# Kernel optimization log

Measured on AMD Instinct MI355X. Metric: run time of the kernel, lower is better.

## Reference

```python
import jax, jax.numpy as jnp
import numpy as np

P = 30000    # pathway graph nodes
E = 480000   # edges
G = 20000    # genes
MP = 32      # max pathways per gene (padded)
R = 28       # pathway root count
B = 4096     # batch of gene pairs
IN, H, OUT = 394, 256, 64
GD = 128     # params.gene_dim


def setup_inputs() -> dict:
    key = jax.random.key(0)
    ks = iter(jax.random.split(key, 48))
    nx = lambda shape, s=1.0: jax.random.normal(next(ks), shape, dtype=jnp.float32) * s
    inp = {}
    inp["x1"] = nx((P, IN))
    inp["x2"] = nx((P, IN))
    inp["edge_src"] = jax.random.randint(next(ks), (E,), 0, P)
    inp["edge_dst"] = jax.random.randint(next(ks), (E,), 0, P)
    inp["edge_weight"] = jax.random.uniform(next(ks), (E,), dtype=jnp.float32)
    for g in ("g1", "g2"):
        inp[g + "_w1"] = nx((IN, H), 0.05); inp[g + "_b1"] = jnp.zeros((H,), jnp.float32)
        inp[g + "_w2"] = nx((H, OUT), 0.05); inp[g + "_b2"] = jnp.zeros((OUT,), jnp.float32)
    inp["pl1_w"] = nx((OUT * R, 256), 0.02); inp["pl1_b"] = jnp.zeros((256,), jnp.float32)
    inp["bn1_g"] = jnp.ones((256,), jnp.float32); inp["bn1_b"] = jnp.zeros((256,), jnp.float32)
    inp["pl2_w"] = nx((256, GD), 0.05); inp["pl2_b"] = jnp.zeros((GD,), jnp.float32)
    inp["bn2_g"] = jnp.ones((GD,), jnp.float32); inp["bn2_b"] = jnp.zeros((GD,), jnp.float32)
    inp["fc_w"] = nx((2 * GD, 256), 0.05); inp["fc_b"] = jnp.zeros((256,), jnp.float32)
    inp["fc1_w"] = nx((256, 128), 0.05); inp["fc1_b"] = jnp.zeros((128,), jnp.float32)
    inp["fc2_w"] = nx((128, 1), 0.05); inp["fc2_b"] = jnp.zeros((1,), jnp.float32)
    inp["pathway_root"] = jax.random.randint(next(ks), (P,), 0, R)
    inp["gene_paths"] = jax.random.randint(next(ks), (G, MP), 0, P)
    inp["gene_paths_mask"] = jax.random.uniform(next(ks), (G, MP)) < 0.7
    inp["head_ids"] = jax.random.randint(next(ks), (B,), 0, G)
    inp["tail_ids"] = jax.random.randint(next(ks), (B,), 0, G)
    return inp


def gcn_conv(x, w, b, src, dst, ew):
    # PyG GCNConv with edge weights + self loops (fill_value=1), symmetric norm.
    h = x @ w
    deg = jnp.zeros((x.shape[0],), x.dtype).at[dst].add(ew) + 1.0
    norm = jax.lax.rsqrt(deg)
    msg = h[src] * (ew * norm[src] * norm[dst])[:, None]
    agg = jnp.zeros_like(h).at[dst].add(msg) + h * (norm * norm)[:, None]
    return agg + b


def pathway_gcn(x, w1, b1, w2, b2, src, dst, ew):
    h = jax.nn.relu(gcn_conv(x, w1, b1, src, dst, ew))  # F.dropout in eval = identity
    return gcn_conv(h, w2, b2, src, dst, ew)


def gene_pathway_feat(s, gene_ids, gene_paths, gene_paths_mask, pathway_root):
    # Vectorized form of the per-gene python-loop gather + per-root sum.
    paths = gene_paths[gene_ids]                      # [B, MP]
    m = gene_paths_mask[gene_ids].astype(s.dtype)     # [B, MP]
    gathered = s[paths]                               # [B, MP, 64]
    oh = jax.nn.one_hot(pathway_root[paths], R, dtype=s.dtype) * m[..., None]
    feat = jnp.einsum('bpr,bpd->brd', oh, gathered)   # segment-sum into roots
    return feat.reshape(paths.shape[0], R * s.shape[1])


def batchnorm(x, g, b, eps=1e-5):
    mu = x.mean(0)
    var = x.var(0)  # biased, as torch BN training
    return g * (x - mu) * jax.lax.rsqrt(var + eps) + b


def reference(x1, x2, edge_src, edge_dst, edge_weight,
              g1_w1, g1_b1, g1_w2, g1_b2, g2_w1, g2_b1, g2_w2, g2_b2,
              pl1_w, pl1_b, bn1_g, bn1_b, pl2_w, pl2_b, bn2_g, bn2_b,
              fc_w, fc_b, fc1_w, fc1_b, fc2_w, fc2_b,
              pathway_root, gene_paths, gene_paths_mask, head_ids, tail_ids):
    out1 = pathway_gcn(x1, g1_w1, g1_b1, g1_w2, g1_b2, edge_src, edge_dst, edge_weight)
    out2 = pathway_gcn(x2, g2_w1, g2_b1, g2_w2, g2_b2, edge_src, edge_dst, edge_weight)
    s = out1 + out2  # original stacks feats from both graphs per pathway, then sums

    def fuse(ids):
        f = gene_pathway_feat(s, ids, gene_paths, gene_paths_mask, pathway_root)
        h = jax.nn.relu(batchnorm(f @ pl1_w + pl1_b, bn1_g, bn1_b))
        return batchnorm(h @ pl2_w + pl2_b, bn2_g, bn2_b)

    fuse_feat = jnp.concatenate([fuse(head_ids), fuse(tail_ids)], axis=1)  # [B, 2*GD]
    final = jax.nn.relu(fuse_feat @ fc_w + fc_b) @ fc1_w + fc1_b
    return jax.nn.relu(final) @ fc2_w + fc2_b  # [B, 1]
```

## Files before the change

kernel.cpp:

```cpp
#include <hip/hip_runtime.h>
#include <cstdint>

typedef __attribute__((ext_vector_type(4))) float f32x4;
typedef __attribute__((ext_vector_type(8))) short s16x8;

__device__ inline unsigned short f2bf(float f) {
    unsigned u = __float_as_uint(f);
    unsigned r = (u + 0x7FFFu + ((u >> 16) & 1u)) >> 16;
    return (unsigned short)r;
}
__device__ inline float b2f(unsigned short h) {
    return __uint_as_float(((unsigned)h) << 16);
}

__device__ inline void gload16(const unsigned short* g, unsigned short* l) {
    __builtin_amdgcn_global_load_lds(
        (const __attribute__((address_space(1))) unsigned int*)g,
        (__attribute__((address_space(3))) unsigned int*)l, 16, 0, 0);
}

struct TD { const float* in; unsigned short* out; int K, N, Kp, ldo; };

__global__ void prep_kernel(const unsigned char* __restrict__ mask, int maskBytes,
                            int* __restrict__ flag, float* __restrict__ zspan, long long zwords,
                            TD d0, TD d1, TD d2, TD d3, TD d4, TD d5, TD d6, TD d7) {
    int y = blockIdx.y;
    if (y == 0) {
        if (blockIdx.x != 0) return;
        __shared__ int isByte, isFloat;
        if (threadIdx.x == 0) { isByte = 0; isFloat = 0; }
        __syncthreads();
        const unsigned* w = (const unsigned*)mask;
        for (int i = threadIdx.x; i < maskBytes / 4; i += blockDim.x) {
            unsigned v = w[i];
            if (v == 0u || v == 1u) continue;
            if (v == 0x3f800000u) isFloat = 1; else isByte = 1;
        }
        __syncthreads();
        if (threadIdx.x == 0) *flag = isFloat ? 2 : (isByte ? 1 : 0);
        return;
    }
    if (y == 1) {
        long long i = (long long)blockIdx.x * 256 + threadIdx.x;
        if (i < zwords) zspan[i] = 0.f;
        return;
    }
    TD d = d0;
    if (y == 3) d = d1; else if (y == 4) d = d2; else if (y == 5) d = d3;
    else if (y == 6) d = d4; else if (y == 7) d = d5; else if (y == 8) d = d6; else if (y == 9) d = d7;
    int idx = blockIdx.x * 256 + threadIdx.x;
    if (idx >= d.N * d.Kp) return;
    int n = idx / d.Kp, k = idx - n * d.Kp;
    d.out[(size_t)n * d.ldo + k] = (k < d.K) ? f2bf(d.in[(size_t)k * d.N + n]) : (unsigned short)0;
}

__global__ void deg_cnt_kernel(const int* __restrict__ dst, const float* __restrict__ ew,
                               float* __restrict__ degw, int* __restrict__ cnt, int E) {
    int e = blockIdx.x * 256 + threadIdx.x;
    if (e >= E) return;
    int d = dst[e];
    unsafeAtomicAdd(&degw[d], ew[e]);
    atomicAdd(&cnt[d], 1);
}

__global__ __launch_bounds__(1024) void norm_scan_kernel(const int* __restrict__ cnt,
                                                         int* __restrict__ rowstart,
                                                         float* __restrict__ degw, int P) {
    int t = threadIdx.x;
    if (blockIdx.x > 0) {
        int i = (blockIdx.x - 1) * 1024 + t;
        if (i < P) degw[i] = rsqrtf(degw[i] + 1.0f);
        return;
    }
    __shared__ int wsum[16];
    __shared__ int carry;
    int lane = t & 63, w = t >> 6;
    if (t == 0) { carry = 0; rowstart[0] = 0; }
    __syncthreads();
    for (int base = 0; base < P; base += 1024) {
        int v = (base + t < P) ? cnt[base + t] : 0;
        int x = v;
#pragma unroll
        for (int off = 1; off < 64; off <<= 1) {
            int y = __shfl_up(x, off);
            if (lane >= off) x += y;
        }
        if (lane == 63) wsum[w] = x;
        __syncthreads();
        if (w == 0) {
            int xs = (lane < 16) ? wsum[lane] : 0;
#pragma unroll
            for (int off = 1; off < 16; off <<= 1) {
                int y = __shfl_up(xs, off);
                if (lane >= off) xs += y;
            }
            if (lane < 16) wsum[lane] = xs;
        }
        __syncthreads();
        int wbase = (w == 0) ? 0 : wsum[w - 1];
        int inc = carry + wbase + x;
        if (base + t < P) rowstart[base + t + 1] = inc;
        __syncthreads();
        if (t == 1023) carry = inc;
        __syncthreads();
    }
}

__global__ void fill_kernel(const int* __restrict__ src, const int* __restrict__ dst,
                            const float* __restrict__ ew, const float* __restrict__ norm,
                            const int* __restrict__ rowstart, int* __restrict__ fill,
                            int* __restrict__ csrc, float* __restrict__ coef, int E) {
    int e = blockIdx.x * 256 + threadIdx.x;
    if (e >= E) return;
    int d = dst[e], sI = src[e];
    int pos = rowstart[d] + atomicAdd(&fill[d], 1);
    csrc[pos] = sI;
    coef[pos] = ew[e] * norm[sI] * norm[d];
}

__global__ __launch_bounds__(256) void conv1_agg_kernel(
    const unsigned short* __restrict__ Hb, const float* __restrict__ norm,
    const int* __restrict__ rowstart, const int* __restrict__ csrc, const float* __restrict__ coef,
    const float* __restrict__ b0, const float* __restrict__ b1,
    unsigned short* __restrict__ out, int P) {
    int node = blockIdx.x * 4 + (threadIdx.x >> 6);
    if (node >= P) return;
    int z = blockIdx.y;
    const unsigned short* H = Hb + (size_t)z * P * 256;
    const float* bias = z ? b1 : b0;
    int lane = threadIdx.x & 63;
    int f4 = lane * 4;
    float nn = norm[node];
    ushort4 hv = *(const ushort4*)(H + (size_t)node * 256 + f4);
    float a0 = b2f(hv.x) * nn * nn, a1 = b2f(hv.y) * nn * nn;
    float a2 = b2f(hv.z) * nn * nn, a3 = b2f(hv.w) * nn * nn;
    int s0 = rowstart[node], s1 = rowstart[node + 1];
    int p = s0;
    for (; p + 4 <= s1; p += 4) {
        int i0 = csrc[p], i1 = csrc[p + 1], i2 = csrc[p + 2], i3 = csrc[p + 3];
        float c0 = coef[p], c1 = coef[p + 1], c2 = coef[p + 2], c3 = coef[p + 3];
        ushort4 v0 = *(const ushort4*)(H + (size_t)i0 * 256 + f4);
        ushort4 v1 = *(const ushort4*)(H + (size_t)i1 * 256 + f4);
        ushort4 v2 = *(const ushort4*)(H + (size_t)i2 * 256 + f4);
        ushort4 v3 = *(const ushort4*)(H + (size_t)i3 * 256 + f4);
        a0 += b2f(v0.x) * c0 + b2f(v1.x) * c1 + b2f(v2.x) * c2 + b2f(v3.x) * c3;
        a1 += b2f(v0.y) * c0 + b2f(v1.y) * c1 + b2f(v2.y) * c2 + b2f(v3.y) * c3;
        a2 += b2f(v0.z) * c0 + b2f(v1.z) * c1 + b2f(v2.z) * c2 + b2f(v3.z) * c3;
        a3 += b2f(v0.w) * c0 + b2f(v1.w) * c1 + b2f(v2.w) * c2 + b2f(v3.w) * c3;
    }
    for (; p < s1; ++p) {
        int i0 = csrc[p];
        float c0 = coef[p];
        ushort4 v0 = *(const ushort4*)(H + (size_t)i0 * 256 + f4);
        a0 += b2f(v0.x) * c0; a1 += b2f(v0.y) * c0; a2 += b2f(v0.z) * c0; a3 += b2f(v0.w) * c0;
    }
    float4 bv = *(const float4*)(bias + f4);
    ushort4 o;
    o.x = f2bf(fmaxf(a0 + bv.x, 0.f));
    o.y = f2bf(fmaxf(a1 + bv.y, 0.f));
    o.z = f2bf(fmaxf(a2 + bv.z, 0.f));
    o.w = f2bf(fmaxf(a3 + bv.w, 0.f));
    *(ushort4*)(out + (size_t)node * 512 + z * 256 + f4) = o;
}

__global__ __launch_bounds__(256) void conv2_agg_kernel(
    const unsigned short* __restrict__ T, const float* __restrict__ norm,
    const int* __restrict__ rowstart, const int* __restrict__ csrc, const float* __restrict__ coef,
    const float* __restrict__ b0, const float* __restrict__ b1,
    float* __restrict__ s, int P) {
    int node = blockIdx.x * 4 + (threadIdx.x >> 6);
    if (node >= P) return;
    int lane = threadIdx.x & 63;
    float nn = norm[node];
    float acc = b2f(T[(size_t)node * 64 + lane]) * nn * nn;
    int s0 = rowstart[node], s1 = rowstart[node + 1];
    int p = s0;
    for (; p + 4 <= s1; p += 4) {
        int i0 = csrc[p], i1 = csrc[p + 1], i2 = csrc[p + 2], i3 = csrc[p + 3];
        float c0 = coef[p], c1 = coef[p + 1], c2 = coef[p + 2], c3 = coef[p + 3];
        acc += b2f(T[(size_t)i0 * 64 + lane]) * c0 + b2f(T[(size_t)i1 * 64 + lane]) * c1 +
               b2f(T[(size_t)i2 * 64 + lane]) * c2 + b2f(T[(size_t)i3 * 64 + lane]) * c3;
    }
    for (; p < s1; ++p) acc += b2f(T[(size_t)csrc[p] * 64 + lane]) * coef[p];
    s[(size_t)node * 64 + lane] = acc + b0[lane] + b1[lane];
}

struct G2 {
    const void* A[2]; const unsigned short* Bt[2]; const float* bias[2];
    float* Cf[2]; unsigned short* Cb[2];
};

template<int BM, int BN, int WM, int WN>
__global__ __launch_bounds__(256) void gemm1_hybrid_kernel(
    const float* __restrict__ x0, const float* __restrict__ x1,
    const unsigned short* __restrict__ Bt0, const unsigned short* __restrict__ Bt1,
    unsigned short* __restrict__ C0, unsigned short* __restrict__ C1,
    int M, int IN, int Kp, int ldc) {
    const int z = blockIdx.z;
    const float* A = z ? x1 : x0;
    const unsigned short* Bt = z ? Bt1 : Bt0;
    unsigned short* Cb = z ? C1 : C0;

    constexpr int LDK = 40;
    __shared__ __align__(16) unsigned short As[BM * LDK];
    __shared__ __align__(16) unsigned short Bs[BN * 32];
    const int t = threadIdx.x, lane = t & 63, wid = t >> 6;
    constexpr int NWC = BN / WN;
    const int wr = wid / NWC, wc = wid % NWC;
    constexpr int MR = WM / 16, NR = WN / 16;
    static_assert((BM / WM) * (BN / WN) == 4, "4 waves");
    constexpr int BI = BN / 64;
    const int row0 = blockIdx.y * BM, col0 = blockIdx.x * BN;
    const int sr = lane >> 2;
    const int sc = ((lane & 3) ^ ((lane >> 3) & 3)) * 8;
    int brow[BI];
#pragma unroll
    for (int i = 0; i < BI; ++i) brow[i] = col0 + (wid * BI + i) * 16 + sr;
    const int ar = t >> 2, akc = (t & 3) * 8;
    int arowg = row0 + ar; if (arowg >= M) arowg = M - 1;
    const float* aptr = A + (size_t)arowg * IN;

    f32x4 acc[MR][NR] = {};
    const int r16 = lane & 15, q = lane >> 4;
    const int kbA = q * 8;
    const int kbB = ((q ^ ((r16 >> 1) & 3)) * 8);

    for (int kt = 0; kt < Kp; kt += 32) {
#pragma unroll
        for (int i = 0; i < BI; ++i)
            gload16(Bt + (size_t)brow[i] * Kp + kt + sc, &Bs[(wid * BI + i) * 512]);
        {
            int kg = kt + akc;
            float v[8];
            if (kg + 8 <= IN) {
                float2 a = *(const float2*)(aptr + kg);
                float2 b = *(const float2*)(aptr + kg + 2);
                float2 c = *(const float2*)(aptr + kg + 4);
                float2 d = *(const float2*)(aptr + kg + 6);
                v[0]=a.x; v[1]=a.y; v[2]=b.x; v[3]=b.y; v[4]=c.x; v[5]=c.y; v[6]=d.x; v[7]=d.y;
            } else {
#pragma unroll
                for (int j = 0; j < 8; ++j) v[j] = (kg + j < IN) ? aptr[kg + j] : 0.f;
            }
            s16x8 w;
#pragma unroll
            for (int j = 0; j < 8; ++j) w[j] = (short)f2bf(v[j]);
            *(s16x8*)&As[ar * LDK + akc] = w;
        }
        __syncthreads();
        s16x8 af[MR], bfr[NR];
#pragma unroll
        for (int m = 0; m < MR; ++m)
            af[m] = *(const s16x8*)&As[(wr * WM + m * 16 + r16) * LDK + kbA];
#pragma unroll
        for (int n = 0; n < NR; ++n)
            bfr[n] = *(const s16x8*)&Bs[(wc * WN + n * 16 + r16) * 32 + kbB];
#pragma unroll
        for (int m = 0; m < MR; ++m)
#pragma unroll
            for (int n = 0; n < NR; ++n)
                acc[m][n] = __builtin_amdgcn_mfma_f32_16x16x32_bf16(af[m], bfr[n], acc[m][n], 0, 0, 0);
        __syncthreads();
    }
#pragma unroll
    for (int m = 0; m < MR; ++m)
#pragma unroll
        for (int n = 0; n < NR; ++n) {
            int col = col0 + wc * WN + n * 16 + r16;
#pragma unroll
            for (int r = 0; r < 4; ++r) {
                int row = row0 + wr * WM + m * 16 + q * 4 + r;
                if (row < M) Cb[(size_t)row * ldc + col] = f2bf(acc[m][n][r]);
            }
        }
}

template<int BM, int BN, int WM, int WN>
__global__ __launch_bounds__(256) void m97s_gemm_kernel(
    G2 g, int M, int Kp, int lda, int ldc, int relu) {
    const int z = blockIdx.z;
    const unsigned short* A = (const unsigned short*)(z ? g.A[1] : g.A[0]);
    const unsigned short* Bt = z ? g.Bt[1] : g.Bt[0];
    const float* bias = z ? g.bias[1] : g.bias[0];
    float* Cf = z ? g.Cf[1] : g.Cf[0];
    unsigned short* Cb = z ? g.Cb[1] : g.Cb[0];

    __shared__ __align__(16) unsigned short As[BM * 32];
    __shared__ __align__(16) unsigned short Bs[BN * 32];
    const int t = threadIdx.x, lane = t & 63, wid = t >> 6;
    constexpr int NWC = BN / WN;
    const int wr = wid / NWC, wc = wid % NWC;
    constexpr int MR = WM / 16, NR = WN / 16;
    static_assert((BM / WM) * (BN / WN) == 4, "4 waves");
    constexpr int AI = BM / 64, BI = BN / 64;
    const int row0 = blockIdx.y * BM, col0 = blockIdx.x * BN;
    const int sr = lane >> 2;
    const int sc = ((lane & 3) ^ ((lane >> 3) & 3)) * 8;
    int arow[AI];
#pragma unroll
    for (int i = 0; i < AI; ++i) {
        int r = row0 + (wid * AI + i) * 16 + sr;
        arow[i] = r < M ? r : M - 1;
    }
    int brow[BI];
#pragma unroll
    for (int i = 0; i < BI; ++i) brow[i] = col0 + (wid * BI + i) * 16 + sr;

    f32x4 acc[MR][NR] = {};
    const int r16 = lane & 15;
    const int kb = (((lane >> 4) ^ ((r16 >> 1) & 3)) * 8);

    for (int kt = 0; kt < Kp; kt += 32) {
#pragma unroll
        for (int i = 0; i < AI; ++i)
            gload16(A + (size_t)arow[i] * lda + kt + sc, &As[(wid * AI + i) * 512]);
#pragma unroll
        for (int i = 0; i < BI; ++i)
            gload16(Bt + (size_t)brow[i] * Kp + kt + sc, &Bs[(wid * BI + i) * 512]);
        __syncthreads();
        s16x8 af[MR], bfr[NR];
#pragma unroll
        for (int m = 0; m < MR; ++m)
            af[m] = *(const s16x8*)&As[(wr * WM + m * 16 + r16) * 32 + kb];
#pragma unroll
        for (int n = 0; n < NR; ++n)
            bfr[n] = *(const s16x8*)&Bs[(wc * WN + n * 16 + r16) * 32 + kb];
#pragma unroll
        for (int m = 0; m < MR; ++m)
#pragma unroll
            for (int n = 0; n < NR; ++n)
                acc[m][n] = __builtin_amdgcn_mfma_f32_16x16x32_bf16(af[m], bfr[n], acc[m][n], 0, 0, 0);
        __syncthreads();
    }
#pragma unroll
    for (int m = 0; m < MR; ++m)
#pragma unroll
        for (int n = 0; n < NR; ++n) {
            int col = col0 + wc * WN + n * 16 + r16;
#pragma unroll
            for (int r = 0; r < 4; ++r) {
                int row = row0 + wr * WM + m * 16 + (lane >> 4) * 4 + r;
                if (row < M) {
                    float v = acc[m][n][r] + (bias ? bias[col] : 0.f);
                    if (relu) v = fmaxf(v, 0.f);
                    if (Cf) Cf[(size_t)row * ldc + col] = v;
                    if (Cb) Cb[(size_t)row * ldc + col] = f2bf(v);
                }
            }
        }
}

template<int BM, int BN, int WM, int WN>
__global__ __launch_bounds__(256) void pl1_stats_kernel(
    G2 g, int M, int Kp, int lda, int ldc, float* __restrict__ statsPart, int C) {
    const int z = blockIdx.z;
    const unsigned short* A = (const unsigned short*)(z ? g.A[1] : g.A[0]);
    const unsigned short* Bt = z ? g.Bt[1] : g.Bt[0];
    const float* bias = z ? g.bias[1] : g.bias[0];
    float* Cf = z ? g.Cf[1] : g.Cf[0];

    __shared__ __align__(16) unsigned short As[BM * 32];
    __shared__ __align__(16) unsigned short Bs[BN * 32];
    const int t = threadIdx.x, lane = t & 63, wid = t >> 6;
    constexpr int NWC = BN / WN;
    const int wr = wid / NWC, wc = wid % NWC;
    constexpr int MR = WM / 16, NR = WN / 16;
    constexpr int AI = BM / 64, BI = BN / 64;
    const int row0 = blockIdx.y * BM, col0 = blockIdx.x * BN;
    const int sr = lane >> 2;
    const int sc = ((lane & 3) ^ ((lane >> 3) & 3)) * 8;
    int arow[AI];
#pragma unroll
    for (int i = 0; i < AI; ++i) {
        int r = row0 + (wid * AI + i) * 16 + sr;
        arow[i] = r < M ? r : M - 1;
    }
    int brow[BI];
#pragma unroll
    for (int i = 0; i < BI; ++i) brow[i] = col0 + (wid * BI + i) * 16 + sr;

    f32x4 acc[MR][NR] = {};
    const int r16 = lane & 15, q = lane >> 4;
    const int kb = ((q ^ ((r16 >> 1) & 3)) * 8);

    for (int kt = 0; kt < Kp; kt += 32) {
#pragma unroll
        for (int i = 0; i < AI; ++i)
            gload16(A + (size_t)arow[i] * lda + kt + sc, &As[(wid * AI + i) * 512]);
#pragma unroll
        for (int i = 0; i < BI; ++i)
            gload16(Bt + (size_t)brow[i] * Kp + kt + sc, &Bs[(wid * BI + i) * 512]);
        __syncthreads();
        s16x8 af[MR], bfr[NR];
#pragma unroll
        for (int m = 0; m < MR; ++m)
            af[m] = *(const s16x8*)&As[(wr * WM + m * 16 + r16) * 32 + kb];
#pragma unroll
        for (int n = 0; n < NR; ++n)
            bfr[n] = *(const s16x8*)&Bs[(wc * WN + n * 16 + r16) * 32 + kb];
#pragma unroll
        for (int m = 0; m < MR; ++m)
#pragma unroll
            for (int n = 0; n < NR; ++n)
                acc[m][n] = __builtin_amdgcn_mfma_f32_16x16x32_bf16(af[m], bfr[n], acc[m][n], 0, 0, 0);
        __syncthreads();
    }
    float* sp = statsPart + (size_t)z * 2 * C;
#pragma unroll
    for (int n = 0; n < NR; ++n) {
        int col = col0 + wc * WN + n * 16 + r16;
        float sm = 0.f, sq = 0.f;
#pragma unroll
        for (int m = 0; m < MR; ++m)
#pragma unroll
            for (int r = 0; r < 4; ++r) {
                int row = row0 + wr * WM + m * 16 + q * 4 + r;
                float v = acc[m][n][r] + bias[col];
                Cf[(size_t)row * ldc + col] = v;
                sm += v; sq += v * v;
            }
        sm += __shfl_xor(sm, 16); sq += __shfl_xor(sq, 16);
        sm += __shfl_xor(sm, 32); sq += __shfl_xor(sq, 32);
        if (lane < 16) {
            unsafeAtomicAdd(&sp[col], sm);
            unsafeAtomicAdd(&sp[C + col], sq);
        }
    }
}

template<int BM, int BN, int WM, int WN>
__global__ __launch_bounds__(256) void pl2_bn_stats_kernel(
    const float* __restrict__ z1, const unsigned short* __restrict__ Bt,
    const float* __restrict__ bias, float* __restrict__ z2,
    const float* __restrict__ bn1part, const float* __restrict__ bn1g, const float* __restrict__ bn1b,
    float* __restrict__ bn2part, int Mrows, int Kp, int ldc) {
    const int z = blockIdx.z;
    const float* A = z1 + (size_t)z * Mrows * Kp;
    float* Cf = z2 + (size_t)z * Mrows * ldc;

    constexpr int LDK = 40;
    __shared__ __align__(16) unsigned short As[BM * LDK];
    __shared__ __align__(16) unsigned short Bs[BN * 32];
    __shared__ float sc1[256], sh1[256];
    const int t = threadIdx.x, lane = t & 63, wid = t >> 6;
    {
        const float* bp = bn1part + (size_t)z * 2 * 256;
        float mu = bp[t] / Mrows;
        float var = bp[256 + t] / Mrows - mu * mu;
        float rstd = rsqrtf(var + 1e-5f);
        float s = rstd * bn1g[t];
        sc1[t] = s; sh1[t] = bn1b[t] - mu * s;
    }
    constexpr int NWC = BN / WN;
    const int wr = wid / NWC, wc = wid % NWC;
    constexpr int MR = WM / 16, NR = WN / 16;
    constexpr int BI = BN / 64;
    const int row0 = blockIdx.y * BM, col0 = blockIdx.x * BN;
    const int sr = lane >> 2;
    const int sc = ((lane & 3) ^ ((lane >> 3) & 3)) * 8;
    int brow[BI];
#pragma unroll
    for (int i = 0; i < BI; ++i) brow[i] = col0 + (wid * BI + i) * 16 + sr;
    const int ar = t >> 2, akc = (t & 3) * 8;
    const float* aptr = A + (size_t)(row0 + ar) * Kp;
    f32x4 acc[MR][NR] = {};
    const int r16 = lane & 15, q = lane >> 4;
    const int kbA = q * 8;
    const int kbB = ((q ^ ((r16 >> 1) & 3)) * 8);
    __syncthreads();

    for (int kt = 0; kt < Kp; kt += 32) {
#pragma unroll
        for (int i = 0; i < BI; ++i)
            gload16(Bt + (size_t)brow[i] * Kp + kt + sc, &Bs[(wid * BI + i) * 512]);
        {
            int kg = kt + akc;
            float4 a = *(const float4*)(aptr + kg);
            float4 b = *(const float4*)(aptr + kg + 4);
            float v[8] = {a.x, a.y, a.z, a.w, b.x, b.y, b.z, b.w};
            s16x8 w;
#pragma unroll
            for (int j = 0; j < 8; ++j)
                w[j] = (short)f2bf(fmaxf(v[j] * sc1[kg + j] + sh1[kg + j], 0.f));
            *(s16x8*)&As[ar * LDK + akc] = w;
        }
        __syncthreads();
        s16x8 af[MR], bfr[NR];
#pragma unroll
        for (int m = 0; m < MR; ++m)
            af[m] = *(const s16x8*)&As[(wr * WM + m * 16 + r16) * LDK + kbA];
#pragma unroll
        for (int n = 0; n < NR; ++n)
            bfr[n] = *(const s16x8*)&Bs[(wc * WN + n * 16 + r16) * 32 + kbB];
#pragma unroll
        for (int m = 0; m < MR; ++m)
#pragma unroll
            for (int n = 0; n < NR; ++n)
                acc[m][n] = __builtin_amdgcn_mfma_f32_16x16x32_bf16(af[m], bfr[n], acc[m][n], 0, 0, 0);
        __syncthreads();
    }
    float* sp = bn2part + (size_t)z * 2 * ldc;
#pragma unroll
    for (int n = 0; n < NR; ++n) {
        int col = col0 + wc * WN + n * 16 + r16;
        float sm = 0.f, sq = 0.f;
#pragma unroll
        for (int m = 0; m < MR; ++m)
#pragma unroll
            for (int r = 0; r < 4; ++r) {
                int row = row0 + wr * WM + m * 16 + q * 4 + r;
                float v = acc[m][n][r] + bias[col];
                Cf[(size_t)row * ldc + col] = v;
                sm += v; sq += v * v;
            }
        sm += __shfl_xor(sm, 16); sq += __shfl_xor(sq, 16);
        sm += __shfl_xor(sm, 32); sq += __shfl_xor(sq, 32);
        if (lane < 16) {
            unsafeAtomicAdd(&sp[col], sm);
            unsafeAtomicAdd(&sp[ldc + col], sq);
        }
    }
}

__global__ __launch_bounds__(64) void gene_feat_kernel(
    const float* __restrict__ S, const int* __restrict__ head, const int* __restrict__ tail,
    const int* __restrict__ gene_paths, const void* __restrict__ mask,
    const int* __restrict__ root, unsigned short* __restrict__ feat, const int* __restrict__ flag,
    int B) {
    __shared__ float lds[28 * 64];
    int lane = threadIdx.x;
#pragma unroll
    for (int i = 0; i < 28; ++i) lds[i * 64 + lane] = 0.f;
    int side = blockIdx.y;
    const int* ids = side ? tail : head;
    int gene = ids[blockIdx.x];
    int fl = *flag;
    const unsigned char* mb = (const unsigned char*)mask;
    const int* mi = (const int*)mask;
    const float* mf = (const float*)mask;
    for (int p = 0; p < 32; ++p) {
        int idx = gene * 32 + p;
        int m = (fl == 0) ? mi[idx] : (fl == 1) ? (int)mb[idx] : (mf[idx] != 0.f);
        if (!m) continue;
        int path = gene_paths[idx];
        int r = root[path];
        lds[r * 64 + lane] += S[(size_t)path * 64 + lane];
    }
    unsigned short* frow = feat + ((size_t)side * B + blockIdx.x) * 1792;
#pragma unroll
    for (int i = 0; i < 28; ++i) frow[i * 64 + lane] = f2bf(lds[i * 64 + lane]);
}

__global__ __launch_bounds__(256) void mlp_tail_kernel(
    const float* __restrict__ z2, const float* __restrict__ bn2part,
    const float* __restrict__ bn2g, const float* __restrict__ bn2b,
    const unsigned short* __restrict__ fct, const float* __restrict__ fc_b,
    const unsigned short* __restrict__ fc1t, const float* __restrict__ fc1_b,
    const float* __restrict__ fc2_w, const float* __restrict__ fc2_b,
    float* __restrict__ out, int B) {
    constexpr int LDK = 40;
    __shared__ __align__(16) unsigned short As[64 * LDK];
    __shared__ __align__(16) unsigned short Bs[256 * 32];
    __shared__ __align__(16) unsigned short T1[64 * 264];
    __shared__ float part[64];
    __shared__ float sc2[256], sh2[256];
    const int t = threadIdx.x, lane = t & 63, wid = t >> 6;
    const int row0 = blockIdx.x * 64;
    const int sr = lane >> 2, sc = ((lane & 3) ^ ((lane >> 3) & 3)) * 8;
    const int r16 = lane & 15, q = lane >> 4;
    const int kbA = q * 8;
    const int kbB = ((q ^ ((r16 >> 1) & 3)) * 8);
    const int ar = t >> 2, akc = (t & 3) * 8;

    {
        int side = t >> 7, cc = t & 127;
        const float* bp = bn2part + (size_t)side * 256;
        float mu = bp[cc] / B;
        float var = bp[128 + cc] / B - mu * mu;
        float rstd = rsqrtf(var + 1e-5f);
        float s = rstd * bn2g[cc];
        sc2[t] = s; sh2[t] = bn2b[cc] - mu * s;
    }
    __syncthreads();

    {
        f32x4 acc[4][4] = {};
        int brow[4];
#pragma unroll
        for (int i = 0; i < 4; ++i) brow[i] = (wid * 4 + i) * 16 + sr;
        for (int kt = 0; kt < 256; kt += 32) {
#pragma unroll
            for (int i = 0; i < 4; ++i)
                gload16(fct + (size_t)brow[i] * 256 + kt + sc, &Bs[(wid * 4 + i) * 512]);
            {
                int c0 = kt + akc;
                int side = c0 >> 7, cc = c0 & 127;
                const float* zr = z2 + ((size_t)side * B + row0 + ar) * 128 + cc;
                float4 a = *(const float4*)zr;
                float4 b = *(const float4*)(zr + 4);
                float v[8] = {a.x, a.y, a.z, a.w, b.x, b.y, b.z, b.w};
                s16x8 w;
#pragma unroll
                for (int j = 0; j < 8; ++j) w[j] = (short)f2bf(v[j] * sc2[c0 + j] + sh2[c0 + j]);
                *(s16x8*)&As[ar * LDK + akc] = w;
            }
            __syncthreads();
            s16x8 af[4], bfr[4];
#pragma unroll
            for (int m = 0; m < 4; ++m) af[m] = *(const s16x8*)&As[(m * 16 + r16) * LDK + kbA];
#pragma unroll
            for (int n = 0; n < 4; ++n) bfr[n] = *(const s16x8*)&Bs[(wid * 64 + n * 16 + r16) * 32 + kbB];
#pragma unroll
            for (int m = 0; m < 4; ++m)
#pragma unroll
                for (int n = 0; n < 4; ++n)
                    acc[m][n] = __builtin_amdgcn_mfma_f32_16x16x32_bf16(af[m], bfr[n], acc[m][n], 0, 0, 0);
            __syncthreads();
        }
#pragma unroll
        for (int m = 0; m < 4; ++m)
#pragma unroll
            for (int n = 0; n < 4; ++n) {
                int col = wid * 64 + n * 16 + r16;
#pragma unroll
                for (int r = 0; r < 4; ++r) {
                    int row = m * 16 + q * 4 + r;
                    T1[row * 264 + col] = f2bf(fmaxf(acc[m][n][r] + fc_b[col], 0.f));
                }
            }
    }
    __syncthreads();
    if (t < 64) part[t] = 0.f;

    f32x4 acc2[4][2] = {};
    {
        int brow[2];
#pragma unroll
        for (int i = 0; i < 2; ++i) brow[i] = (wid * 2 + i) * 16 + sr;
        for (int kt = 0; kt < 256; kt += 32) {
#pragma unroll
            for (int i = 0; i < 2; ++i)
                gload16(fc1t + (size_t)brow[i] * 256 + kt + sc, &Bs[(wid * 2 + i) * 512]);
            __syncthreads();
            s16x8 af[4], bfr[2];
#pragma unroll
            for (int m = 0; m < 4; ++m) af[m] = *(const s16x8*)&T1[(m * 16 + r16) * 264 + kt + q * 8];
#pragma unroll
            for (int n = 0; n < 2; ++n) bfr[n] = *(const s16x8*)&Bs[(wid * 32 + n * 16 + r16) * 32 + kbB];
#pragma unroll
            for (int m = 0; m < 4; ++m)
#pragma unroll
                for (int n = 0; n < 2; ++n)
                    acc2[m][n] = __builtin_amdgcn_mfma_f32_16x16x32_bf16(af[m], bfr[n], acc2[m][n], 0, 0, 0);
            __syncthreads();
        }
    }
#pragma unroll
    for (int m = 0; m < 4; ++m)
#pragma unroll
        for (int r = 0; r < 4; ++r) {
            float sv = 0.f;
#pragma unroll
            for (int n = 0; n < 2; ++n) {
                int col = wid * 32 + n * 16 + r16;
                float v = fmaxf(acc2[m][n][r] + fc1_b[col], 0.f);
                sv += v * fc2_w[col];
            }
#pragma unroll
            for (int off = 1; off < 16; off <<= 1) sv += __shfl_xor(sv, off);
            if (r16 == 0) atomicAdd(&part[m * 16 + q * 4 + r], sv);
        }
    __syncthreads();
    if (t < 64 && row0 + t < B) out[row0 + t] = part[t] + fc2_b[0];
}

extern "C" void kernel_launch(void* const* d_in, const int* in_sizes, int n_in,
                              void* d_out, int out_size, void* d_ws, size_t ws_size,
                              hipStream_t stream) {
    const float* x[2] = {(const float*)d_in[0], (const float*)d_in[1]};
    const int* esrc = (const int*)d_in[2];
    const int* edst = (const int*)d_in[3];
    const float* ew = (const float*)d_in[4];
    const float* g_w1[2] = {(const float*)d_in[5], (const float*)d_in[9]};
    const float* g_b1[2] = {(const float*)d_in[6], (const float*)d_in[10]};
    const float* g_w2[2] = {(const float*)d_in[7], (const float*)d_in[11]};
    const float* g_b2[2] = {(const float*)d_in[8], (const float*)d_in[12]};
    const float* pl1_w = (const float*)d_in[13];
    const float* pl1_b = (const float*)d_in[14];
    const float* bn1_g = (const float*)d_in[15];
    const float* bn1_b = (const float*)d_in[16];
    const float* pl2_w = (const float*)d_in[17];
    const float* pl2_b = (const float*)d_in[18];
    const float* bn2_g = (const float*)d_in[19];
    const float* bn2_b = (const float*)d_in[20];
    const float* fc_w = (const float*)d_in[21];
    const float* fc_b = (const float*)d_in[22];
    const float* fc1_w = (const float*)d_in[23];
    const float* fc1_b = (const float*)d_in[24];
    const float* fc2_w = (const float*)d_in[25];
    const float* fc2_b = (const float*)d_in[26];
    const int* root = (const int*)d_in[27];
    const int* gene_paths = (const int*)d_in[28];
    const void* gmask = d_in[29];
    const int* head = (const int*)d_in[30];
    const int* tail = (const int*)d_in[31];

    const int P = in_sizes[27];
    const int E = in_sizes[2];
    const int B = in_sizes[30];
    const int IN = 394, Kp1 = 416, H = 256, OUT = 64, GD = 128;
    const int MB = (P + 63) / 64;

    char* ws = (char*)d_ws;
    size_t off = 0;
    auto alloc = [&](size_t bytes) -> char* {
        char* p = ws + off;
        off = (off + bytes + 255) & ~(size_t)255;
        return p;
    };
    int* flag = (int*)alloc(256);
    float* norm = (float*)alloc((size_t)P * 4);
    int* cnt = (int*)alloc((size_t)P * 4);
    int* fillp = (int*)alloc((size_t)P * 4);
    float* bn1part = (float*)alloc((size_t)2 * 2 * 256 * 4);
    float* bn2part = (float*)alloc((size_t)2 * 2 * 128 * 4);
    char* zend = ws + off;
    int* rowstart = (int*)alloc((size_t)(P + 1) * 4);
    int* csrc = (int*)alloc((size_t)E * 4);
    float* coef = (float*)alloc((size_t)E * 4);
    unsigned short* W1t = (unsigned short*)alloc((size_t)2 * H * Kp1 * 2);
    unsigned short* W2tc = (unsigned short*)alloc((size_t)OUT * 512 * 2);
    unsigned short* pl1t = (unsigned short*)alloc((size_t)256 * 1792 * 2);
    unsigned short* pl2t = (unsigned short*)alloc((size_t)GD * 256 * 2);
    unsigned short* fct = (unsigned short*)alloc((size_t)256 * 256 * 2);
    unsigned short* fc1t = (unsigned short*)alloc((size_t)GD * 256 * 2);
    unsigned short* bufH = (unsigned short*)alloc((size_t)2 * P * H * 2);
    unsigned short* bufh1 = (unsigned short*)alloc((size_t)P * 512 * 2);
    float* s = (float*)alloc((size_t)P * OUT * 4);
    (void)n_in; (void)out_size; (void)ws_size;

    unsigned short* bufh2 = bufH;
    unsigned short* feat = bufh1;
    char* mlp = (char*)bufH + 4194304;
    size_t mo = 0;
    auto malloc2 = [&](size_t bytes) -> char* {
        char* p = mlp + mo;
        mo = (mo + bytes + 255) & ~(size_t)255;
        return p;
    };
    float* z1 = (float*)malloc2((size_t)2 * B * 256 * 4);
    float* z2 = (float*)malloc2((size_t)2 * B * GD * 4);

    {
        long long zwords = (zend - (char*)norm) / 4;
        TD d0 = {g_w1[0], W1t, IN, H, Kp1, Kp1};
        TD d1 = {g_w1[1], W1t + (size_t)H * Kp1, IN, H, Kp1, Kp1};
        TD d2 = {g_w2[0], W2tc, H, OUT, H, 512};
        TD d3 = {g_w2[1], W2tc + 256, H, OUT, H, 512};
        TD d4 = {pl1_w, pl1t, 1792, 256, 1792, 1792};
        TD d5 = {pl2_w, pl2t, 256, GD, 256, 256};
        TD d6 = {fc_w, fct, 256, 256, 256, 256};
        TD d7 = {fc1_w, fc1t, 256, GD, 256, 256};
        prep_kernel<<<dim3(1792, 10), 256, 0, stream>>>(
            (const unsigned char*)gmask, 4096, flag, norm, zwords,
            d0, d1, d2, d3, d4, d5, d6, d7);
    }

    deg_cnt_kernel<<<(E + 255) / 256, 256, 0, stream>>>(edst, ew, norm, cnt, E);
    norm_scan_kernel<<<1 + (P + 1023) / 1024, 1024, 0, stream>>>(cnt, rowstart, norm, P);
    fill_kernel<<<(E + 255) / 256, 256, 0, stream>>>(esrc, edst, ew, norm, rowstart, fillp, csrc, coef, E);

    gemm1_hybrid_kernel<64, 256, 64, 64><<<dim3(1, MB, 2), 256, 0, stream>>>(
        x[0], x[1], W1t, W1t + (size_t)H * Kp1, bufH, bufH + (size_t)P * H, P, IN, Kp1, H);

    conv1_agg_kernel<<<dim3((P + 3) / 4, 2), 256, 0, stream>>>(bufH, norm, rowstart, csrc, coef,
                                                               g_b1[0], g_b1[1], bufh1, P);
    {
        G2 g = {{bufh1, nullptr}, {W2tc, nullptr}, {nullptr, nullptr},
                {nullptr, nullptr}, {bufh2, nullptr}};
        m97s_gemm_kernel<64, 64, 32, 32><<<dim3(1, MB, 1), 256, 0, stream>>>(
            g, P, 512, 512, OUT, 0);
    }
    conv2_agg_kernel<<<dim3((P + 3) / 4), 256, 0, stream>>>(bufh2, norm, rowstart, csrc, coef,
                                                            g_b2[0], g_b2[1], s, P);

    gene_feat_kernel<<<dim3(B, 2), 64, 0, stream>>>(s, head, tail, gene_paths, gmask, root, feat, flag, B);

    {
        G2 g = {{feat, feat + (size_t)B * 1792}, {pl1t, pl1t}, {pl1_b, pl1_b},
                {z1, z1 + (size_t)B * 256}, {nullptr, nullptr}};
        pl1_stats_kernel<64, 128, 32, 64><<<dim3(2, B / 64, 2), 256, 0, stream>>>(
            g, B, 1792, 1792, 256, bn1part, 256);
    }
    pl2_bn_stats_kernel<64, 64, 32, 32><<<dim3(2, B / 64, 2), 256, 0, stream>>>(
        z1, pl2t, pl2_b, z2, bn1part, bn1_g, bn1_b, bn2part, B, 256, GD);

    mlp_tail_kernel<<<B / 64, 256, 0, stream>>>(z2, bn2part, bn2_g, bn2_b, fct, fc_b,
                                                fc1t, fc1_b, fc2_w, fc2_b, (float*)d_out, B);
}
```

Measured before the change: 346.1 us.

## Double-buffer LDS tiles in GEMM kernels to overlap loads with MFMA

```diff
diff --git a/kernel.cpp b/kernel.cpp
--- a/kernel.cpp
+++ b/kernel.cpp
@@ -82,8 +82,8 @@
         int x = v;
 #pragma unroll
         for (int off = 1; off < 64; off <<= 1) {
-            int y = __shfl_up(x, off);
-            if (lane >= off) x += y;
+            int y2 = __shfl_up(x, off);
+            if (lane >= off) x += y2;
         }
         if (lane == 63) wsum[w] = x;
         __syncthreads();
@@ -91,8 +91,8 @@
             int xs = (lane < 16) ? wsum[lane] : 0;
 #pragma unroll
             for (int off = 1; off < 16; off <<= 1) {
-                int y = __shfl_up(xs, off);
-                if (lane >= off) xs += y;
+                int y2 = __shfl_up(xs, off);
+                if (lane >= off) xs += y2;
             }
             if (lane < 16) wsum[lane] = xs;
         }
@@ -202,8 +202,8 @@
     unsigned short* Cb = z ? C1 : C0;
 
     constexpr int LDK = 40;
-    __shared__ __align__(16) unsigned short As[BM * LDK];
-    __shared__ __align__(16) unsigned short Bs[BN * 32];
+    __shared__ __align__(16) unsigned short As[2][BM * LDK];
+    __shared__ __align__(16) unsigned short Bs[2][BN * 32];
     const int t = threadIdx.x, lane = t & 63, wid = t >> 6;
     constexpr int NWC = BN / WN;
     const int wr = wid / NWC, wc = wid % NWC;
@@ -225,42 +225,57 @@
     const int kbA = q * 8;
     const int kbB = ((q ^ ((r16 >> 1) & 3)) * 8);
 
+    auto stageB = [&](int buf, int kt) {
+#pragma unroll
+        for (int i = 0; i < BI; ++i)
+            gload16(Bt + (size_t)brow[i] * Kp + kt + sc, &Bs[buf][(wid * BI + i) * 512]);
+    };
+    auto loadA = [&](int kt, float* v) {
+        int kg = kt + akc;
+        if (kg + 8 <= IN) {
+            float2 a = *(const float2*)(aptr + kg);
+            float2 b = *(const float2*)(aptr + kg + 2);
+            float2 c = *(const float2*)(aptr + kg + 4);
+            float2 d = *(const float2*)(aptr + kg + 6);
+            v[0]=a.x; v[1]=a.y; v[2]=b.x; v[3]=b.y; v[4]=c.x; v[5]=c.y; v[6]=d.x; v[7]=d.y;
+        } else {
+#pragma unroll
+            for (int j = 0; j < 8; ++j) v[j] = (kg + j < IN) ? aptr[kg + j] : 0.f;
+        }
+    };
+    auto writeA = [&](int buf, const float* v) {
+        s16x8 w;
+#pragma unroll
+        for (int j = 0; j < 8; ++j) w[j] = (short)f2bf(v[j]);
+        *(s16x8*)&As[buf][ar * LDK + akc] = w;
+    };
+
+    {
+        float v[8];
+        stageB(0, 0);
+        loadA(0, v);
+        writeA(0, v);
+    }
+    int cur = 0;
     for (int kt = 0; kt < Kp; kt += 32) {
-#pragma unroll
-        for (int i = 0; i < BI; ++i)
-            gload16(Bt + (size_t)brow[i] * Kp + kt + sc, &Bs[(wid * BI + i) * 512]);
-        {
-            int kg = kt + akc;
-            float v[8];
-            if (kg + 8 <= IN) {
-                float2 a = *(const float2*)(aptr + kg);
-                float2 b = *(const float2*)(aptr + kg + 2);
-                float2 c = *(const float2*)(aptr + kg + 4);
-                float2 d = *(const float2*)(aptr + kg + 6);
-                v[0]=a.x; v[1]=a.y; v[2]=b.x; v[3]=b.y; v[4]=c.x; v[5]=c.y; v[6]=d.x; v[7]=d.y;
-            } else {
-#pragma unroll
-                for (int j = 0; j < 8; ++j) v[j] = (kg + j < IN) ? aptr[kg + j] : 0.f;
-            }
-            s16x8 w;
-#pragma unroll
-            for (int j = 0; j < 8; ++j) w[j] = (short)f2bf(v[j]);
-            *(s16x8*)&As[ar * LDK + akc] = w;
-        }
-        __syncthreads();
+        __syncthreads();
+        float nv[8];
+        const bool has = (kt + 32 < Kp);
+        if (has) { stageB(cur ^ 1, kt + 32); loadA(kt + 32, nv); }
         s16x8 af[MR], bfr[NR];
 #pragma unroll
         for (int m = 0; m < MR; ++m)
-            af[m] = *(const s16x8*)&As[(wr * WM + m * 16 + r16) * LDK + kbA];
+            af[m] = *(const s16x8*)&As[cur][(wr * WM + m * 16 + r16) * LDK + kbA];
 #pragma unroll
         for (int n = 0; n < NR; ++n)
-            bfr[n] = *(const s16x8*)&Bs[(wc * WN + n * 16 + r16) * 32 + kbB];
+            bfr[n] = *(const s16x8*)&Bs[cur][(wc * WN + n * 16 + r16) * 32 + kbB];
 #pragma unroll
         for (int m = 0; m < MR; ++m)
 #pragma unroll
             for (int n = 0; n < NR; ++n)
                 acc[m][n] = __builtin_amdgcn_mfma_f32_16x16x32_bf16(af[m], bfr[n], acc[m][n], 0, 0, 0);
-        __syncthreads();
+        if (has) writeA(cur ^ 1, nv);
+        cur ^= 1;
     }
 #pragma unroll
     for (int m = 0; m < MR; ++m)
@@ -285,8 +300,8 @@
     float* Cf = z ? g.Cf[1] : g.Cf[0];
     unsigned short* Cb = z ? g.Cb[1] : g.Cb[0];
 
-    __shared__ __align__(16) unsigned short As[BM * 32];
-    __shared__ __align__(16) unsigned short Bs[BN * 32];
+    __shared__ __align__(16) unsigned short As[2][BM * 32];
+    __shared__ __align__(16) unsigned short Bs[2][BN * 32];
     const int t = threadIdx.x, lane = t & 63, wid = t >> 6;
     constexpr int NWC = BN / WN;
     const int wr = wid / NWC, wc = wid % NWC;
@@ -310,27 +325,33 @@
     const int r16 = lane & 15;
     const int kb = (((lane >> 4) ^ ((r16 >> 1) & 3)) * 8);
 
+    auto stage = [&](int buf, int kt) {
+#pragma unroll
+        for (int i = 0; i < AI; ++i)
+            gload16(A + (size_t)arow[i] * lda + kt + sc, &As[buf][(wid * AI + i) * 512]);
+#pragma unroll
+        for (int i = 0; i < BI; ++i)
+            gload16(Bt + (size_t)brow[i] * Kp + kt + sc, &Bs[buf][(wid * BI + i) * 512]);
+    };
+
+    stage(0, 0);
+    int cur = 0;
     for (int kt = 0; kt < Kp; kt += 32) {
-#pragma unroll
-        for (int i = 0; i < AI; ++i)
-            gload16(A + (size_t)arow[i] * lda + kt + sc, &As[(wid * AI + i) * 512]);
-#pragma unroll
-        for (int i = 0; i < BI; ++i)
-            gload16(Bt + (size_t)brow[i] * Kp + kt + sc, &Bs[(wid * BI + i) * 512]);
-        __syncthreads();
+        __syncthreads();
+        if (kt + 32 < Kp) stage(cur ^ 1, kt + 32);
         s16x8 af[MR], bfr[NR];
 #pragma unroll
         for (int m = 0; m < MR; ++m)
-            af[m] = *(const s16x8*)&As[(wr * WM + m * 16 + r16) * 32 + kb];
+            af[m] = *(const s16x8*)&As[cur][(wr * WM + m * 16 + r16) * 32 + kb];
 #pragma unroll
         for (int n = 0; n < NR; ++n)
-            bfr[n] = *(const s16x8*)&Bs[(wc * WN + n * 16 + r16) * 32 + kb];
+            bfr[n] = *(const s16x8*)&Bs[cur][(wc * WN + n * 16 + r16) * 32 + kb];
 #pragma unroll
         for (int m = 0; m < MR; ++m)
 #pragma unroll
             for (int n = 0; n < NR; ++n)
                 acc[m][n] = __builtin_amdgcn_mfma_f32_16x16x32_bf16(af[m], bfr[n], acc[m][n], 0, 0, 0);
-        __syncthreads();
+        cur ^= 1;
     }
 #pragma unroll
     for (int m = 0; m < MR; ++m)
@@ -359,8 +380,8 @@
     const float* bias = z ? g.bias[1] : g.bias[0];
     float* Cf = z ? g.Cf[1] : g.Cf[0];
 
-    __shared__ __align__(16) unsigned short As[BM * 32];
-    __shared__ __align__(16) unsigned short Bs[BN * 32];
+    __shared__ __align__(16) unsigned short As[2][BM * 32];
+    __shared__ __align__(16) unsigned short Bs[2][BN * 32];
     const int t = threadIdx.x, lane = t & 63, wid = t >> 6;
     constexpr int NWC = BN / WN;
     const int wr = wid / NWC, wc = wid % NWC;
@@ -383,27 +404,33 @@
     const int r16 = lane & 15, q = lane >> 4;
     const int kb = ((q ^ ((r16 >> 1) & 3)) * 8);
 
+    auto stage = [&](int buf, int kt) {
+#pragma unroll
+        for (int i = 0; i < AI; ++i)
+            gload16(A + (size_t)arow[i] * lda + kt + sc, &As[buf][(wid * AI + i) * 512]);
+#pragma unroll
+        for (int i = 0; i < BI; ++i)
+            gload16(Bt + (size_t)brow[i] * Kp + kt + sc, &Bs[buf][(wid * BI + i) * 512]);
+    };
+
+    stage(0, 0);
+    int cur = 0;
     for (int kt = 0; kt < Kp; kt += 32) {
-#pragma unroll
-        for (int i = 0; i < AI; ++i)
-            gload16(A + (size_t)arow[i] * lda + kt + sc, &As[(wid * AI + i) * 512]);
-#pragma unroll
-        for (int i = 0; i < BI; ++i)
-            gload16(Bt + (size_t)brow[i] * Kp + kt + sc, &Bs[(wid * BI + i) * 512]);
-        __syncthreads();
+        __syncthreads();
+        if (kt + 32 < Kp) stage(cur ^ 1, kt + 32);
         s16x8 af[MR], bfr[NR];
 #pragma unroll
         for (int m = 0; m < MR; ++m)
-            af[m] = *(const s16x8*)&As[(wr * WM + m * 16 + r16) * 32 + kb];
+            af[m] = *(const s16x8*)&As[cur][(wr * WM + m * 16 + r16) * 32 + kb];
 #pragma unroll
         for (int n = 0; n < NR; ++n)
-            bfr[n] = *(const s16x8*)&Bs[(wc * WN + n * 16 + r16) * 32 + kb];
+            bfr[n] = *(const s16x8*)&Bs[cur][(wc * WN + n * 16 + r16) * 32 + kb];
 #pragma unroll
         for (int m = 0; m < MR; ++m)
 #pragma unroll
             for (int n = 0; n < NR; ++n)
                 acc[m][n] = __builtin_amdgcn_mfma_f32_16x16x32_bf16(af[m], bfr[n], acc[m][n], 0, 0, 0);
-        __syncthreads();
+        cur ^= 1;
     }
     float* sp = statsPart + (size_t)z * 2 * C;
 #pragma unroll
```

After: 348.8 us. About the same (+0.8%).
